# Kernel optimization log

Measured on AMD Instinct MI355X. Metric: run time of the kernel, lower is better.

The kernel has to match this reference:

```python
import math
import jax, jax.numpy as jnp
import numpy as np

N_EMBD = 768
N_HEAD = 12
BLOCK_SIZE = 1024
B, T, N_ENC = 8, 1024, 257
EPS = 1e-5


def _ln(x, g, b):
    m = jnp.mean(x, axis=-1, keepdims=True)
    v = jnp.var(x, axis=-1, keepdims=True)
    return (x - m) * jax.lax.rsqrt(v + EPS) * g + b


def _heads(t, n_head):
    B_, N_, C_ = t.shape
    return t.reshape(B_, N_, n_head, C_ // n_head).transpose(0, 2, 1, 3)  # [B,H,N,D]


def setup_inputs() -> dict:
    key = jax.random.key(0)
    ks = jax.random.split(key, 16)
    s = 0.02
    d, h4, dq = N_EMBD, 4 * N_EMBD, N_EMBD // 4
    inp = {
        'x': jax.random.normal(ks[0], (B, T, d), jnp.float32),
        'x_enc': jax.random.normal(ks[1], (B, N_ENC, d), jnp.float32),
        'ln1_g': jnp.ones((d,), jnp.float32), 'ln1_b': jnp.zeros((d,), jnp.float32),
        'ln2_g': jnp.ones((d,), jnp.float32), 'ln2_b': jnp.zeros((d,), jnp.float32),
        'ln3_g': jnp.ones((d,), jnp.float32), 'ln3_b': jnp.zeros((d,), jnp.float32),
        'attn_w': jax.random.normal(ks[2], (d, 3 * d), jnp.float32) * s,
        'attn_bias': jnp.zeros((3 * d,), jnp.float32),
        'attn_proj_w': jax.random.normal(ks[3], (d, d), jnp.float32) * s,
        'attn_proj_b': jnp.zeros((d,), jnp.float32),
        'img_w': jax.random.normal(ks[4], (d, 2 * d), jnp.float32) * s,
        'img_b': jnp.zeros((2 * d,), jnp.float32),
        'cap_w': jax.random.normal(ks[5], (d, d), jnp.float32) * s,
        'cap_b': jnp.zeros((d,), jnp.float32),
        'cross_proj_w': jax.random.normal(ks[6], (d, d), jnp.float32) * s,
        'cross_proj_b': jnp.zeros((d,), jnp.float32),
        'ad1_w': jax.random.normal(ks[7], (d, dq), jnp.float32) * s,
        'ad1_b': jnp.zeros((dq,), jnp.float32),
        'ad2_w': jax.random.normal(ks[8], (dq, d), jnp.float32) * s,
        'ad2_b': jnp.zeros((d,), jnp.float32),
        'fc_w': jax.random.normal(ks[9], (d, h4), jnp.float32) * s,
        'fc_b': jnp.zeros((h4,), jnp.float32),
        'mproj_w': jax.random.normal(ks[10], (h4, d), jnp.float32) * s,
        'mproj_b': jnp.zeros((d,), jnp.float32),
    }
    return inp


def _block(x, x_enc, ln1_g, ln1_b, ln2_g, ln2_b, ln3_g, ln3_b,
           attn_w, attn_bias, attn_proj_w, attn_proj_b,
           img_w, img_b, cap_w, cap_b, cross_proj_w, cross_proj_b,
           ad1_w, ad1_b, ad2_w, ad2_b, fc_w, fc_b, mproj_w, mproj_b):
    d, nh = N_EMBD, N_HEAD
    hd = d // nh
    scale = 1.0 / math.sqrt(hd)

    def adapter(h):
        return jax.nn.relu(h @ ad1_w + ad1_b) @ ad2_w + ad2_b

    # --- causal self-attention ---
    h = _ln(x, ln1_g, ln1_b)
    qkv = h @ attn_w + attn_bias
    q, k, v = jnp.split(qkv, 3, axis=2)
    q, k, v = _heads(q, nh), _heads(k, nh), _heads(v, nh)  # [B,H,T,hd]
    att = jnp.einsum('bhqd,bhkd->bhqk', q, k) * scale
    Tq = x.shape[1]
    causal = jnp.tril(jnp.ones((Tq, Tq), bool))
    att = jnp.where(causal, att, -jnp.inf)
    att = jax.nn.softmax(att, axis=-1)
    sa = jnp.einsum('bhqk,bhkd->bhqd', att, v).transpose(0, 2, 1, 3).reshape(x.shape)
    sa = sa @ attn_proj_w + attn_proj_b
    x = x + adapter(sa)

    # --- cross-attention (queries from x, keys/values from x_enc) ---
    hq = _ln(x, ln1_g, ln1_b)
    he = _ln(x_enc, ln3_g, ln3_b)
    kv = he @ img_w + img_b
    k2, v2 = jnp.split(kv, 2, axis=2)
    q2 = hq @ cap_w + cap_b
    q2, k2, v2 = _heads(q2, nh), _heads(k2, nh), _heads(v2, nh)
    catt = jax.nn.softmax(jnp.einsum('bhqd,bhkd->bhqk', q2, k2) * scale, axis=-1)
    ca = jnp.einsum('bhqk,bhkd->bhqd', catt, v2).transpose(0, 2, 1, 3).reshape(x.shape)
    ca = ca @ cross_proj_w + cross_proj_b
    x = x + adapter(ca)

    # --- MLP ---
    hm = _ln(x, ln2_g, ln2_b)
    m = jax.nn.gelu(hm @ fc_w + fc_b, approximate=True) @ mproj_w + mproj_b
    x = x + adapter(m)
    return x, x_enc


def reference(x, x_enc, ln1_g, ln1_b, ln2_g, ln2_b, ln3_g, ln3_b,
              attn_w, attn_bias, attn_proj_w, attn_proj_b,
              img_w, img_b, cap_w, cap_b, cross_proj_w, cross_proj_b,
              ad1_w, ad1_b, ad2_w, ad2_b, fc_w, fc_b, mproj_w, mproj_b):
    return _block(x, x_enc, ln1_g, ln1_b, ln2_g, ln2_b, ln3_g, ln3_b,
                  attn_w, attn_bias, attn_proj_w, attn_proj_b,
                  img_w, img_b, cap_w, cap_b, cross_proj_w, cross_proj_b,
                  ad1_w, ad1_b, ad2_w, ad2_b, fc_w, fc_b, mproj_w, mproj_b)
```

## Files before the change

### kernel.cpp

```cpp
#include <hip/hip_runtime.h>

typedef unsigned short u16;
typedef short bf16x8 __attribute__((ext_vector_type(8)));
typedef float f32x4 __attribute__((ext_vector_type(4)));
typedef unsigned short u16x4 __attribute__((ext_vector_type(4)));

__device__ __forceinline__ u16 f2bf(float f) {
  union { float f; unsigned u; } v; v.f = f;
  unsigned u = v.u;
  unsigned r = (u + 0x7FFFu + ((u >> 16) & 1u)) >> 16;
  return (u16)r;
}
__device__ __forceinline__ float bf2f(u16 h) {
  union { unsigned u; float f; } v; v.u = ((unsigned)h) << 16;
  return v.f;
}
__device__ __forceinline__ unsigned cvt_pk_bf16(float lo, float hi) {
  unsigned d;
  asm("v_cvt_pk_bf16_f32 %0, %1, %2" : "=v"(d) : "v"(lo), "v"(hi));
  return d;
}
__device__ __forceinline__ float gelu_f(float x) {
  const float c1 = -2.302585093f;
  const float c2 = -0.1029620967f;
  float t = __builtin_fmaf(x * x, c2, c1) * x;
  float e = exp2f(t);
  return x * __builtin_amdgcn_rcpf(e + 1.0f);
}

#define GLD_LDS16(gp, lp)                                             \
  __builtin_amdgcn_global_load_lds(                                   \
      (const __attribute__((address_space(1))) void*)(gp),            \
      (__attribute__((address_space(3))) void*)(lp), 16, 0, 0)

template<int OFF>
__device__ __forceinline__ u16x4 tr16(unsigned a) {
  u16x4 d;
  asm volatile("ds_read_b64_tr_b16 %0, %1 offset:%2" : "=&v"(d) : "v"(a), "n"(OFF));
  return d;
}
__device__ __forceinline__ bf16x8 pack8(u16x4 a, u16x4 b) {
  union { u16x4 p[2]; bf16x8 v; } u;
  u.p[0] = a; u.p[1] = b;
  return u.v;
}
__device__ __forceinline__ u16x4 pack4(unsigned w0, unsigned w1) {
  union { unsigned w[2]; u16x4 v; } u;
  u.w[0] = w0; u.w[1] = w1;
  return u.v;
}

struct TrBatch {
  const float* W[9];
  u16* Bt[9];
  int K[9], N[9], Kpad[9], Npad[9];
  int tstart[10];
};
__global__ __launch_bounds__(256)
void transpose_all(TrBatch tb) {
  __shared__ float tile[64][65];
  const int tid = blockIdx.x;
  int mi = 0;
  while (mi < 8 && tid >= tb.tstart[mi + 1]) ++mi;
  const int lt = tid - tb.tstart[mi];
  const int tx = tb.Npad[mi] >> 6;
  const int n0 = (lt % tx) * 64;
  const int k0 = (lt / tx) * 64;
  const float* W = tb.W[mi];
  u16* Bt = tb.Bt[mi];
  const int K = tb.K[mi], N = tb.N[mi], Kpad = tb.Kpad[mi];
  const int t = threadIdx.x;
  const int c = t & 63;
  const int rb = t >> 6;
#pragma unroll
  for (int i = 0; i < 16; ++i) {
    int r = i * 4 + rb;
    float v = 0.f;
    if (k0 + r < K && n0 + c < N) v = W[(size_t)(k0 + r) * N + n0 + c];
    tile[r][c] = v;
  }
  __syncthreads();
#pragma unroll
  for (int i = 0; i < 16; ++i) {
    int r = i * 4 + rb;
    Bt[(size_t)(n0 + r) * Kpad + k0 + c] = f2bf(tile[c][r]);
  }
}

__global__ __launch_bounds__(64)
void ln_kernel(const float* __restrict__ X, const float* __restrict__ G,
               const float* __restrict__ Bv, u16* __restrict__ O, int Mreal) {
  const int row = blockIdx.x;
  const int l = threadIdx.x;
  u16* op = O + (size_t)row * 768;
  if (row >= Mreal) {
    u16x4 z = {0, 0, 0, 0};
#pragma unroll
    for (int i = 0; i < 3; ++i) *(u16x4*)(op + (i * 64 + l) * 4) = z;
    return;
  }
  const float* xp = X + (size_t)row * 768;
  float v[12];
  float s = 0.f, s2 = 0.f;
#pragma unroll
  for (int i = 0; i < 3; ++i) {
    float4 t4 = *(const float4*)(xp + (i * 64 + l) * 4);
    v[i * 4 + 0] = t4.x; v[i * 4 + 1] = t4.y; v[i * 4 + 2] = t4.z; v[i * 4 + 3] = t4.w;
    s += t4.x + t4.y + t4.z + t4.w;
    s2 += t4.x * t4.x + t4.y * t4.y + t4.z * t4.z + t4.w * t4.w;
  }
#pragma unroll
  for (int off = 32; off > 0; off >>= 1) {
    s += __shfl_xor(s, off);
    s2 += __shfl_xor(s2, off);
  }
  const float mean = s * (1.0f / 768.0f);
  const float var = s2 * (1.0f / 768.0f) - mean * mean;
  const float rstd = rsqrtf(var + 1e-5f);
#pragma unroll
  for (int i = 0; i < 3; ++i) {
    int base = (i * 64 + l) * 4;
    float4 g4 = *(const float4*)(G + base);
    float4 b4 = *(const float4*)(Bv + base);
    u16x4 o4;
    o4[0] = f2bf((v[i * 4 + 0] - mean) * rstd * g4.x + b4.x);
    o4[1] = f2bf((v[i * 4 + 1] - mean) * rstd * g4.y + b4.y);
    o4[2] = f2bf((v[i * 4 + 2] - mean) * rstd * g4.z + b4.z);
    o4[3] = f2bf((v[i * 4 + 3] - mean) * rstd * g4.w + b4.w);
    *(u16x4*)(op + base) = o4;
  }
}

template<bool DOLN, bool RESID>
__global__ __launch_bounds__(64)
void resid_ln(const float* __restrict__ S, float* __restrict__ D,
              const u16* __restrict__ P,
              const float* __restrict__ G, const float* __restrict__ Bv,
              u16* __restrict__ O) {
  const int row = blockIdx.x;
  const int l = threadIdx.x;
  const float* sp = S + (size_t)row * 768;
  float* dp = D + (size_t)row * 768;
  float v[12];
  float s = 0.f, s2 = 0.f;
#pragma unroll
  for (int i = 0; i < 3; ++i) {
    const int base = (i * 64 + l) * 4;
    float4 t4 = *(const float4*)(sp + base);
    if (RESID) {
      u16x4 p4 = *(const u16x4*)(P + (size_t)row * 768 + base);
      t4.x += bf2f(p4[0]); t4.y += bf2f(p4[1]);
      t4.z += bf2f(p4[2]); t4.w += bf2f(p4[3]);
    }
    v[i * 4 + 0] = t4.x; v[i * 4 + 1] = t4.y; v[i * 4 + 2] = t4.z; v[i * 4 + 3] = t4.w;
    s += t4.x + t4.y + t4.z + t4.w;
    s2 += t4.x * t4.x + t4.y * t4.y + t4.z * t4.z + t4.w * t4.w;
    *(float4*)(dp + base) = t4;
  }
  if (DOLN) {
#pragma unroll
    for (int off = 32; off > 0; off >>= 1) {
      s += __shfl_xor(s, off);
      s2 += __shfl_xor(s2, off);
    }
    const float mean = s * (1.0f / 768.0f);
    const float var = s2 * (1.0f / 768.0f) - mean * mean;
    const float rstd = rsqrtf(var + 1e-5f);
    u16* op = O + (size_t)row * 768;
#pragma unroll
    for (int i = 0; i < 3; ++i) {
      int base = (i * 64 + l) * 4;
      float4 g4 = *(const float4*)(G + base);
      float4 b4 = *(const float4*)(Bv + base);
      u16x4 o4;
      o4[0] = f2bf((v[i * 4 + 0] - mean) * rstd * g4.x + b4.x);
      o4[1] = f2bf((v[i * 4 + 1] - mean) * rstd * g4.y + b4.y);
      o4[2] = f2bf((v[i * 4 + 2] - mean) * rstd * g4.z + b4.z);
      o4[3] = f2bf((v[i * 4 + 3] - mean) * rstd * g4.w + b4.w);
      *(u16x4*)(op + base) = o4;
    }
  }
}

template<int MODE>
__global__ void gemm_bt(const u16* __restrict__ A, const u16* __restrict__ Bt,
                        void* __restrict__ C, const float* __restrict__ bias,
                        int K, int ldc, int nbias) {
  __shared__ u16 As[2 * 128 * 32];
  __shared__ u16 Bs[2 * 128 * 32];
  const int t = threadIdx.x;
  const int lane = t & 63;
  const int wid = t >> 6;
  const int wm = (wid >> 1) * 64;
  const int wn = (wid & 1) * 64;
  const int tm = blockIdx.x * 128;
  const int tn = blockIdx.y * 128;

  f32x4 zero = {0.f, 0.f, 0.f, 0.f};
  f32x4 acc[4][4];
#pragma unroll
  for (int i = 0; i < 4; ++i)
#pragma unroll
    for (int j = 0; j < 4; ++j) acc[i][j] = zero;

  const int rowA = lane & 15;
  const int kb = (((lane >> 4) ^ ((rowA >> 1) & 3)) << 3);
  const int kTiles = K >> 6;
  for (int kt = 0; kt < kTiles; ++kt) {
    const int kk = kt << 6;
#pragma unroll
    for (int i = 0; i < 4; ++i) {
      const int c = i * 256 + t;
      const int r = (c >> 2) & 127;
      const int cc = ((c >> 9) << 5) + ((((c & 3) ^ ((r >> 1) & 3))) << 3);
      GLD_LDS16(A + (size_t)(tm + r) * K + kk + cc, As + c * 8);
      GLD_LDS16(Bt + (size_t)(tn + r) * K + kk + cc, Bs + c * 8);
    }
    __syncthreads();
#pragma unroll
    for (int ks = 0; ks < 2; ++ks) {
      bf16x8 af[4], bfr[4];
      const int base = ks * 4096;
#pragma unroll
      for (int i = 0; i < 4; ++i) {
        af[i] = *(const bf16x8*)(As + base + (wm + i * 16 + rowA) * 32 + kb);
        bfr[i] = *(const bf16x8*)(Bs + base + (wn + i * 16 + rowA) * 32 + kb);
      }
#pragma unroll
      for (int mi = 0; mi < 4; ++mi)
#pragma unroll
        for (int ni = 0; ni < 4; ++ni)
          acc[mi][ni] = __builtin_amdgcn_mfma_f32_16x16x32_bf16(af[mi], bfr[ni], acc[mi][ni], 0, 0, 0);
    }
    __syncthreads();
  }
  const int col0 = lane & 15;
  const int row0 = (lane >> 4) << 2;
#pragma unroll
  for (int mi = 0; mi < 4; ++mi) {
#pragma unroll
    for (int ni = 0; ni < 4; ++ni) {
      int col = tn + wn + ni * 16 + col0;
      float bb = (col < nbias) ? bias[col] : 0.f;
      float vv[4];
#pragma unroll
      for (int r = 0; r < 4; ++r) {
        float v = acc[mi][ni][r] + bb;
        if (MODE == 1) v = fmaxf(v, 0.f);
        else if (MODE == 2) v = gelu_f(v);
        vv[r] = v;
      }
      unsigned w0 = cvt_pk_bf16(vv[0], vv[1]);
      unsigned w1 = cvt_pk_bf16(vv[2], vv[3]);
      size_t row = (size_t)(tm + wm + mi * 16 + row0);
      u16* cp = (u16*)C + row * ldc + col;
      cp[0] = (u16)w0;
      cp[(size_t)ldc] = (u16)(w0 >> 16);
      cp[(size_t)ldc * 2] = (u16)w1;
      cp[(size_t)ldc * 3] = (u16)(w1 >> 16);
    }
  }
}

template<int MODE>
__global__ __launch_bounds__(256)
void gemm_bt_m64(const u16* __restrict__ A, const u16* __restrict__ Bt,
                 void* __restrict__ C, const float* __restrict__ bias,
                 int K, int ldc, int nbias) {
  __shared__ u16 As[2 * 64 * 32];
  __shared__ u16 Bs[2 * 128 * 32];
  const int t = threadIdx.x;
  const int lane = t & 63;
  const int wid = t >> 6;
  const int wn = wid * 32;
  const int tm = blockIdx.x * 64;
  const int tn = blockIdx.y * 128;

  f32x4 zero = {0.f, 0.f, 0.f, 0.f};
  f32x4 acc[4][2];
#pragma unroll
  for (int i = 0; i < 4; ++i)
#pragma unroll
    for (int j = 0; j < 2; ++j) acc[i][j] = zero;

  const int rowA = lane & 15;
  const int kb = (((lane >> 4) ^ ((rowA >> 1) & 3)) << 3);
  const int kTiles = K >> 6;
  for (int kt = 0; kt < kTiles; ++kt) {
    const int kk = kt << 6;
#pragma unroll
    for (int i = 0; i < 2; ++i) {
      const int c = i * 256 + t;
      const int r = (c >> 2) & 63;
      const int cc = ((c >> 8) << 5) + ((((c & 3) ^ ((r >> 1) & 3))) << 3);
      GLD_LDS16(A + (size_t)(tm + r) * K + kk + cc, As + c * 8);
    }
#pragma unroll
    for (int i = 0; i < 4; ++i) {
      const int c = i * 256 + t;
      const int r = (c >> 2) & 127;
      const int cc = ((c >> 9) << 5) + ((((c & 3) ^ ((r >> 1) & 3))) << 3);
      GLD_LDS16(Bt + (size_t)(tn + r) * K + kk + cc, Bs + c * 8);
    }
    __syncthreads();
#pragma unroll
    for (int ks = 0; ks < 2; ++ks) {
      bf16x8 af[4], bfr[2];
#pragma unroll
      for (int i = 0; i < 4; ++i)
        af[i] = *(const bf16x8*)(As + ks * 2048 + (i * 16 + rowA) * 32 + kb);
#pragma unroll
      for (int j = 0; j < 2; ++j)
        bfr[j] = *(const bf16x8*)(Bs + ks * 4096 + (wn + j * 16 + rowA) * 32 + kb);
#pragma unroll
      for (int mi = 0; mi < 4; ++mi)
#pragma unroll
        for (int ni = 0; ni < 2; ++ni)
          acc[mi][ni] = __builtin_amdgcn_mfma_f32_16x16x32_bf16(af[mi], bfr[ni], acc[mi][ni], 0, 0, 0);
    }
    __syncthreads();
  }
  const int col0 = lane & 15;
  const int row0 = (lane >> 4) << 2;
#pragma unroll
  for (int mi = 0; mi < 4; ++mi) {
#pragma unroll
    for (int ni = 0; ni < 2; ++ni) {
      int col = tn + wn + ni * 16 + col0;
      float bb = (col < nbias) ? bias[col] : 0.f;
      float vv[4];
#pragma unroll
      for (int r = 0; r < 4; ++r) {
        float v = acc[mi][ni][r] + bb;
        if (MODE == 1) v = fmaxf(v, 0.f);
        vv[r] = v;
      }
      unsigned w0 = cvt_pk_bf16(vv[0], vv[1]);
      unsigned w1 = cvt_pk_bf16(vv[2], vv[3]);
      size_t row = (size_t)(tm + mi * 16 + row0);
      u16* cp = (u16*)C + row * ldc + col;
      cp[0] = (u16)w0;
      cp[(size_t)ldc] = (u16)(w0 >> 16);
      cp[(size_t)ldc * 2] = (u16)w1;
      cp[(size_t)ldc * 3] = (u16)(w1 >> 16);
    }
  }
}

struct GemmJob {
  const u16* A; const u16* Bt; u16* C; const float* bias;
  int K, ldc, nbias, mblocks;
};
__global__ __launch_bounds__(256)
void gemm_bt_dual(GemmJob j0, GemmJob j1, int split) {
  __shared__ u16 As[2 * 128 * 32];
  __shared__ u16 Bs[2 * 128 * 32];
  const int bid = blockIdx.x;
  const GemmJob& J = (bid < split) ? j0 : j1;
  const int lb = (bid < split) ? bid : bid - split;
  const int tm = (lb % J.mblocks) * 128;
  const int tn = (lb / J.mblocks) * 128;
  const u16* A = J.A;
  const u16* Bt = J.Bt;
  const int K = J.K;

  const int t = threadIdx.x;
  const int lane = t & 63;
  const int wid = t >> 6;
  const int wm = (wid >> 1) * 64;
  const int wn = (wid & 1) * 64;

  f32x4 zero = {0.f, 0.f, 0.f, 0.f};
  f32x4 acc[4][4];
#pragma unroll
  for (int i = 0; i < 4; ++i)
#pragma unroll
    for (int j = 0; j < 4; ++j) acc[i][j] = zero;

  const int rowA = lane & 15;
  const int kb = (((lane >> 4) ^ ((rowA >> 1) & 3)) << 3);
  const int kTiles = K >> 6;
  for (int kt = 0; kt < kTiles; ++kt) {
    const int kk = kt << 6;
#pragma unroll
    for (int i = 0; i < 4; ++i) {
      const int c = i * 256 + t;
      const int r = (c >> 2) & 127;
      const int cc = ((c >> 9) << 5) + ((((c & 3) ^ ((r >> 1) & 3))) << 3);
      GLD_LDS16(A + (size_t)(tm + r) * K + kk + cc, As + c * 8);
      GLD_LDS16(Bt + (size_t)(tn + r) * K + kk + cc, Bs + c * 8);
    }
    __syncthreads();
#pragma unroll
    for (int ks = 0; ks < 2; ++ks) {
      bf16x8 af[4], bfr[4];
      const int base = ks * 4096;
#pragma unroll
      for (int i = 0; i < 4; ++i) {
        af[i] = *(const bf16x8*)(As + base + (wm + i * 16 + rowA) * 32 + kb);
        bfr[i] = *(const bf16x8*)(Bs + base + (wn + i * 16 + rowA) * 32 + kb);
      }
#pragma unroll
      for (int mi = 0; mi < 4; ++mi)
#pragma unroll
        for (int ni = 0; ni < 4; ++ni)
          acc[mi][ni] = __builtin_amdgcn_mfma_f32_16x16x32_bf16(af[mi], bfr[ni], acc[mi][ni], 0, 0, 0);
    }
    __syncthreads();
  }
  const int col0 = lane & 15;
  const int row0 = (lane >> 4) << 2;
#pragma unroll
  for (int mi = 0; mi < 4; ++mi) {
#pragma unroll
    for (int ni = 0; ni < 4; ++ni) {
      int col = tn + wn + ni * 16 + col0;
      float bb = (col < J.nbias) ? J.bias[col] : 0.f;
      unsigned w0 = cvt_pk_bf16(acc[mi][ni][0] + bb, acc[mi][ni][1] + bb);
      unsigned w1 = cvt_pk_bf16(acc[mi][ni][2] + bb, acc[mi][ni][3] + bb);
      size_t row = (size_t)(tm + wm + mi * 16 + row0);
      u16* cp = J.C + row * J.ldc + col;
      cp[0] = (u16)w0;
      cp[(size_t)J.ldc] = (u16)(w0 >> 16);
      cp[(size_t)J.ldc * 2] = (u16)w1;
      cp[(size_t)J.ldc * 3] = (u16)(w1 >> 16);
    }
  }
}

template<bool CAUSAL>
__global__ __launch_bounds__(256)
void attn_mfma(const u16* __restrict__ Q, const u16* __restrict__ Kp,
               const u16* __restrict__ Vp,
               u16* __restrict__ O0, u16* __restrict__ O1, float2* __restrict__ ML,
               int seqkv, int qrs, int krs,
               long long qBatch, long long kBatch,
               int qoff, int koff, int voff) {
  __shared__ __align__(16) u16 Ks[64 * 64];
  __shared__ __align__(16) u16 Vs[4096];
  __shared__ __align__(16) u16 Ps[4][1024];
  const int t = threadIdx.x;
  const int lane = t & 63;
  const int wid = t >> 6;
  const int b = blockIdx.x / 12, h = blockIdx.x % 12;
  const int yq = CAUSAL ? ((int)gridDim.y - 1 - (int)blockIdx.y) : (int)blockIdx.y;
  const int q0 = yq * 64;
  const int colid = lane & 15;
  const int rgrp = lane >> 4;
  const int z = CAUSAL ? blockIdx.z : 0;

  int kt_begin = 0, kt_end;
  if (CAUSAL) {
    const int ntr = yq + 1;
    const int half = (ntr + 1) >> 1;
    kt_begin = z ? half : 0;
    kt_end = z ? ntr : half;
  } else {
    kt_end = (seqkv + 63) >> 6;
  }
  u16* Op = (CAUSAL && z) ? O1 : O0;

  if (CAUSAL && kt_begin >= kt_end) {
    if (colid == 0) {
#pragma unroll
      for (int r = 0; r < 4; ++r) {
        int qrow = q0 + wid * 16 + rgrp * 4 + r;
        ML[((size_t)z * 8192 + b * 1024 + qrow) * 12 + h] = make_float2(-1e30f, 0.f);
      }
    }
    return;
  }

  const u16* qp = Q + (size_t)b * qBatch + qoff + (size_t)(q0 + wid * 16 + colid) * qrs + h * 64;
  bf16x8 qa[2];
#pragma unroll
  for (int s = 0; s < 2; ++s) qa[s] = *(const bf16x8*)(qp + s * 32 + (rgrp << 3));

  f32x4 oacc[4];
#pragma unroll
  for (int i = 0; i < 4; ++i) oacc[i] = (f32x4){0.f, 0.f, 0.f, 0.f};
  float m[4] = {-1e30f, -1e30f, -1e30f, -1e30f};
  float l[4] = {0.f, 0.f, 0.f, 0.f};

  const u16* kbase = Kp + (size_t)b * kBatch + koff + h * 64;
  const u16* vbase = Vp + (size_t)b * kBatch + voff + h * 64;

  const int srr = t >> 3, sdc = t & 7;
  int kwo[2], vwo[2];
#pragma unroll
  for (int i = 0; i < 2; ++i) {
    const int r = srr + 32 * i;
    kwo[i] = r * 64 + ((sdc ^ (r & 7)) << 3);
    vwo[i] = ((sdc >> 1) << 10) + (i << 9) + (((srr >> 2) & 1) << 8)
           + (((srr >> 3) & 3) << 6) + ((srr & 3) << 4) + (((2 * sdc) & 3) << 2);
  }
  const unsigned vs_base = (unsigned)(size_t)&Vs[0] + 8u * (unsigned)lane;
  const unsigned ps_base = (unsigned)(size_t)&Ps[wid][0] + 8u * (unsigned)lane;

  bf16x8 kz[2], vz[2];
  auto LOADT = [&](int kt) {
    const int k0 = kt * 64;
#pragma unroll
    for (int i = 0; i < 2; ++i) {
      const int tk = k0 + srr + 32 * i;
      const int dc = sdc << 3;
      kz[i] = (bf16x8){0, 0, 0, 0, 0, 0, 0, 0};
      vz[i] = (bf16x8){0, 0, 0, 0, 0, 0, 0, 0};
      if (tk < seqkv) {
        kz[i] = *(const bf16x8*)(kbase + (size_t)tk * krs + dc);
        vz[i] = *(const bf16x8*)(vbase + (size_t)tk * krs + dc);
      }
    }
  };
  LOADT(kt_begin);

  constexpr float SC2 = 0.18033688011112042f;

  for (int kt = kt_begin; kt < kt_end; ++kt) {
    const int k0 = kt * 64;
#pragma unroll
    for (int i = 0; i < 2; ++i) {
      *(bf16x8*)&Ks[kwo[i]] = kz[i];
      *(bf16x8*)&Vs[vwo[i]] = vz[i];
    }
    __syncthreads();
    if (kt + 1 < kt_end) LOADT(kt + 1);

    f32x4 sacc[4];
#pragma unroll
    for (int c = 0; c < 4; ++c) sacc[c] = (f32x4){0.f, 0.f, 0.f, 0.f};
#pragma unroll
    for (int c = 0; c < 4; ++c)
#pragma unroll
      for (int s = 0; s < 2; ++s) {
        bf16x8 kf = *(const bf16x8*)&Ks[(c * 16 + colid) * 64 +
                                        ((((s << 2) + rgrp) ^ (colid & 7)) << 3)];
        sacc[c] = __builtin_amdgcn_mfma_f32_16x16x32_bf16(qa[s], kf, sacc[c], 0, 0, 0);
      }

    const bool domask = CAUSAL ? (kt == yq) : (kt == kt_end - 1);
    if (domask) {
#pragma unroll
      for (int c = 0; c < 4; ++c) {
        int kv = k0 + c * 16 + colid;
#pragma unroll
        for (int r = 0; r < 4; ++r) {
          int q = q0 + wid * 16 + rgrp * 4 + r;
          if ((CAUSAL && kv > q) || (!CAUSAL && kv >= seqkv)) sacc[c][r] = -1e30f;
        }
      }
    }

    float pms[4];
#pragma unroll
    for (int r = 0; r < 4; ++r) {
      float v = fmaxf(fmaxf(sacc[0][r], sacc[1][r]), fmaxf(sacc[2][r], sacc[3][r]));
#pragma unroll
      for (int off = 1; off < 16; off <<= 1) v = fmaxf(v, __shfl_xor(v, off));
      pms[r] = v * SC2;
    }
    bool ok = (pms[0] <= m[0] + 8.f) && (pms[1] <= m[1] + 8.f) &&
              (pms[2] <= m[2] + 8.f) && (pms[3] <= m[3] + 8.f);
    if (!__all(ok)) {
#pragma unroll
      for (int r = 0; r < 4; ++r) {
        float newm = fmaxf(m[r], pms[r]);
        float corr = exp2f(m[r] - newm);
        m[r] = newm;
        l[r] *= corr;
#pragma unroll
        for (int dc2 = 0; dc2 < 4; ++dc2) oacc[dc2][r] *= corr;
      }
    }

    float pv[4][4];
    float psum[4] = {0.f, 0.f, 0.f, 0.f};
#pragma unroll
    for (int c = 0; c < 4; ++c)
#pragma unroll
      for (int r = 0; r < 4; ++r) {
        float p = exp2f(__builtin_fmaf(sacc[c][r], SC2, -m[r]));
        pv[c][r] = p;
        psum[r] += p;
      }
#pragma unroll
    for (int r = 0; r < 4; ++r) {
#pragma unroll
      for (int off = 1; off < 16; off <<= 1) psum[r] += __shfl_xor(psum[r], off);
      l[r] += psum[r];
    }

#pragma unroll
    for (int c = 0; c < 4; ++c) {
      unsigned w0 = cvt_pk_bf16(pv[c][0], pv[c][1]);
      unsigned w1 = cvt_pk_bf16(pv[c][2], pv[c][3]);
      const int pa = ((c >> 1) << 9) + (((colid >> 2) & 1) << 8)
                   + (((2 * c + (colid >> 3)) & 3) << 6) + ((colid & 3) << 4) + (rgrp << 2);
      *(u16x4*)&Ps[wid][pa] = pack4(w0, w1);
    }
    __builtin_amdgcn_sched_barrier(0);

    u16x4 p00 = tr16<0>(ps_base);
    u16x4 p01 = tr16<512>(ps_base);
    u16x4 p10 = tr16<1024>(ps_base);
    u16x4 p11 = tr16<1536>(ps_base);
    asm volatile("s_waitcnt lgkmcnt(0)" ::: "memory");
    __builtin_amdgcn_sched_barrier(0);
    bf16x8 pf0 = pack8(p00, p01);
    bf16x8 pf1 = pack8(p10, p11);

#pragma unroll
    for (int dc2 = 0; dc2 < 4; ++dc2) {
      const unsigned va = vs_base + (unsigned)(dc2 * 2048);
      u16x4 v00 = tr16<0>(va);
      u16x4 v01 = tr16<512>(va);
      u16x4 v10 = tr16<1024>(va);
      u16x4 v11 = tr16<1536>(va);
      asm volatile("s_waitcnt lgkmcnt(0)" ::: "memory");
      __builtin_amdgcn_sched_barrier(0);
      bf16x8 vf0 = pack8(v00, v01);
      bf16x8 vf1 = pack8(v10, v11);
      oacc[dc2] = __builtin_amdgcn_mfma_f32_16x16x32_bf16(pf0, vf0, oacc[dc2], 0, 0, 0);
      oacc[dc2] = __builtin_amdgcn_mfma_f32_16x16x32_bf16(pf1, vf1, oacc[dc2], 0, 0, 0);
    }
    __syncthreads();
  }

#pragma unroll
  for (int r = 0; r < 4; ++r) {
    int qrow = q0 + wid * 16 + rgrp * 4 + r;
    u16* op = Op + ((size_t)b * 1024 + qrow) * 768 + h * 64;
    if (CAUSAL) {
      unsigned w0 = cvt_pk_bf16(oacc[0][r], oacc[1][r]);
      unsigned w1 = cvt_pk_bf16(oacc[2][r], oacc[3][r]);
      op[colid] = (u16)w0;
      op[16 + colid] = (u16)(w0 >> 16);
      op[32 + colid] = (u16)w1;
      op[48 + colid] = (u16)(w1 >> 16);
      if (colid == 0)
        ML[((size_t)z * 8192 + b * 1024 + qrow) * 12 + h] = make_float2(m[r], l[r]);
    } else {
      float inv = 1.f / l[r];
      unsigned w0 = cvt_pk_bf16(oacc[0][r] * inv, oacc[1][r] * inv);
      unsigned w1 = cvt_pk_bf16(oacc[2][r] * inv, oacc[3][r] * inv);
      op[colid] = (u16)w0;
      op[16 + colid] = (u16)(w0 >> 16);
      op[32 + colid] = (u16)w1;
      op[48 + colid] = (u16)(w1 >> 16);
    }
  }
}

__global__ __launch_bounds__(64)
void attn_combine(const u16* __restrict__ P0, const u16* __restrict__ P1,
                  const float2* __restrict__ ML, u16* __restrict__ O) {
  const int row = blockIdx.x;
  const int l = threadIdx.x;
#pragma unroll
  for (int i = 0; i < 3; ++i) {
    const int base = (i * 64 + l) * 4;
    const int h = base >> 6;
    float2 ml0 = ML[(size_t)row * 12 + h];
    float2 ml1 = ML[(size_t)8192 * 12 + row * 12 + h];
    float mm = fmaxf(ml0.x, ml1.x);
    float w0 = exp2f(ml0.x - mm);
    float w1 = exp2f(ml1.x - mm);
    float inv = 1.f / (ml0.y * w0 + ml1.y * w1);
    u16x4 a = *(const u16x4*)(P0 + (size_t)row * 768 + base);
    u16x4 c = *(const u16x4*)(P1 + (size_t)row * 768 + base);
    u16x4 o4;
#pragma unroll
    for (int j = 0; j < 4; ++j)
      o4[j] = f2bf((bf2f(a[j]) * w0 + bf2f(c[j]) * w1) * inv);
    *(u16x4*)(O + (size_t)row * 768 + base) = o4;
  }
}

extern "C" void kernel_launch(void* const* d_in, const int* in_sizes, int n_in,
                              void* d_out, int out_size, void* d_ws, size_t ws_size,
                              hipStream_t stream) {
  const float* x        = (const float*)d_in[0];
  const float* x_enc    = (const float*)d_in[1];
  const float* ln1_g    = (const float*)d_in[2];
  const float* ln1_b    = (const float*)d_in[3];
  const float* ln2_g    = (const float*)d_in[4];
  const float* ln2_b    = (const float*)d_in[5];
  const float* ln3_g    = (const float*)d_in[6];
  const float* ln3_b    = (const float*)d_in[7];
  const float* attn_w   = (const float*)d_in[8];
  const float* attn_bias= (const float*)d_in[9];
  const float* proj_w   = (const float*)d_in[10];
  const float* proj_b   = (const float*)d_in[11];
  const float* img_w    = (const float*)d_in[12];
  const float* img_b    = (const float*)d_in[13];
  const float* cap_w    = (const float*)d_in[14];
  const float* cap_b    = (const float*)d_in[15];
  const float* cross_w  = (const float*)d_in[16];
  const float* cross_b  = (const float*)d_in[17];
  const float* ad1_w    = (const float*)d_in[18];
  const float* ad1_b    = (const float*)d_in[19];
  const float* ad2_w    = (const float*)d_in[20];
  const float* ad2_b    = (const float*)d_in[21];
  const float* fc_w     = (const float*)d_in[22];
  const float* fc_b     = (const float*)d_in[23];
  const float* mproj_w  = (const float*)d_in[24];
  const float* mproj_b  = (const float*)d_in[25];

  const int Mx = 8192;
  const int Me = 2056;
  const int MeP = 2176;

  float* out_x  = (float*)d_out;
  float* out_xe = out_x + (size_t)Mx * 768;

  char* ws = (char*)d_ws;
  size_t off = 0;
  auto alloc = [&](size_t elems) {
    u16* p = (u16*)(ws + off);
    off = (off + elems * 2 + 255) & ~(size_t)255;
    return p;
  };
  u16* wt_attn  = alloc((size_t)2304 * 768);
  u16* wt_proj  = alloc((size_t)768 * 768);
  u16* wt_img   = alloc((size_t)1536 * 768);
  u16* wt_cap   = alloc((size_t)768 * 768);
  u16* wt_cross = alloc((size_t)768 * 768);
  u16* wt_ad1   = alloc((size_t)256 * 768);
  u16* wt_ad2   = alloc((size_t)768 * 256);
  u16* wt_fc    = alloc((size_t)3072 * 768);
  u16* wt_mproj = alloc((size_t)768 * 3072);
  u16* hbuf     = alloc((size_t)Mx * 768);
  u16* big      = alloc((size_t)Mx * 3072);
  u16* p0       = alloc((size_t)Mx * 768);
  u16* p1       = alloc((size_t)Mx * 768);
  u16* hid      = alloc((size_t)Mx * 256);
  float2* mlbuf = (float2*)alloc((size_t)2 * 8192 * 12 * 4);
  u16* q2  = big;
  u16* kvb = big + (size_t)Mx * 768;

  hipMemcpyAsync(out_xe, x_enc, (size_t)Me * 768 * 4, hipMemcpyDeviceToDevice, stream);

  TrBatch tb;
  int nt = 0;
  tb.tstart[0] = 0;
  auto addT = [&](const float* W, u16* Bt, int K, int N, int Kp, int Np) {
    tb.W[nt] = W; tb.Bt[nt] = Bt; tb.K[nt] = K; tb.N[nt] = N;
    tb.Kpad[nt] = Kp; tb.Npad[nt] = Np;
    tb.tstart[nt + 1] = tb.tstart[nt] + (Np / 64) * (Kp / 64);
    ++nt;
  };
  addT(attn_w, wt_attn, 768, 2304, 768, 2304);
  addT(proj_w, wt_proj, 768, 768, 768, 768);
  addT(img_w, wt_img, 768, 1536, 768, 1536);
  addT(cap_w, wt_cap, 768, 768, 768, 768);
  addT(cross_w, wt_cross, 768, 768, 768, 768);
  addT(ad1_w, wt_ad1, 768, 192, 768, 256);
  addT(ad2_w, wt_ad2, 192, 768, 256, 768);
  addT(fc_w, wt_fc, 768, 3072, 768, 3072);
  addT(mproj_w, wt_mproj, 3072, 768, 3072, 768);
  transpose_all<<<tb.tstart[9], 256, 0, stream>>>(tb);

  auto GEMM = [&](const u16* A, const u16* Bt, void* C, const float* bias,
                  int M, int N, int K, int ldc, int nbias, int mode) {
    dim3 g(M / 128, N / 128);
    if (mode == 0)      gemm_bt<0><<<g, 256, 0, stream>>>(A, Bt, C, bias, K, ldc, nbias);
    else if (mode == 1) gemm_bt<1><<<g, 256, 0, stream>>>(A, Bt, C, bias, K, ldc, nbias);
    else                gemm_bt<2><<<g, 256, 0, stream>>>(A, Bt, C, bias, K, ldc, nbias);
  };
  auto GEMM_M64 = [&](const u16* A, const u16* Bt, void* C, const float* bias,
                      int M, int N, int K, int ldc, int nbias, int mode) {
    dim3 g(M / 64, N / 128);
    if (mode == 0) gemm_bt_m64<0><<<g, 256, 0, stream>>>(A, Bt, C, bias, K, ldc, nbias);
    else           gemm_bt_m64<1><<<g, 256, 0, stream>>>(A, Bt, C, bias, K, ldc, nbias);
  };
  auto ADAPTER = [&](const u16* in, u16* padw) {
    GEMM_M64(in, wt_ad1, hid, ad1_b, Mx, 256, 768, 256, 192, 1);
    GEMM_M64(hid, wt_ad2, padw, ad2_b, Mx, 768, 256, 768, 768, 0);
  };

  resid_ln<true, false><<<Mx, 64, 0, stream>>>(x, out_x, nullptr, ln1_g, ln1_b, hbuf);

  GEMM(hbuf, wt_attn, big, attn_bias, Mx, 2304, 768, 2304, 2304, 0);
  attn_mfma<true><<<dim3(96, 16, 2), 256, 0, stream>>>(
      big, big, big, hbuf, p1, mlbuf, 1024, 2304, 2304,
      (long long)1024 * 2304, (long long)1024 * 2304, 0, 768, 1536);
  attn_combine<<<Mx, 64, 0, stream>>>(hbuf, p1, mlbuf, p0);
  GEMM_M64(p0, wt_proj, p1, proj_b, Mx, 768, 768, 768, 768, 0);
  ADAPTER(p1, p0);
  resid_ln<true, true><<<Mx, 64, 0, stream>>>(out_x, out_x, p0, ln1_g, ln1_b, hbuf);

  ln_kernel<<<MeP, 64, 0, stream>>>(x_enc, ln3_g, ln3_b, p0, Me);
  {
    GemmJob jkv = { p0,   wt_img, kvb, img_b, 768, 1536, 1536, MeP / 128 };
    GemmJob jq2 = { hbuf, wt_cap, q2,  cap_b, 768, 768,  768,  Mx / 128 };
    const int split = (MeP / 128) * (1536 / 128);
    const int total = split + (Mx / 128) * (768 / 128);
    gemm_bt_dual<<<total, 256, 0, stream>>>(jkv, jq2, split);
  }
  attn_mfma<false><<<dim3(96, 16), 256, 0, stream>>>(
      q2, kvb, kvb, p1, nullptr, nullptr, 257, 768, 1536,
      (long long)1024 * 768, (long long)257 * 1536, 0, 0, 768);
  GEMM_M64(p1, wt_cross, p0, cross_b, Mx, 768, 768, 768, 768, 0);
  ADAPTER(p0, p1);
  resid_ln<true, true><<<Mx, 64, 0, stream>>>(out_x, out_x, p1, ln2_g, ln2_b, hbuf);

  GEMM(hbuf, wt_fc, big, fc_b, Mx, 3072, 768, 3072, 3072, 2);
  GEMM_M64(big, wt_mproj, p0, mproj_b, Mx, 768, 3072, 768, 768, 0);
  ADAPTER(p0, p1);
  resid_ln<false, true><<<Mx, 64, 0, stream>>>(out_x, out_x, p1, nullptr, nullptr, nullptr);

  (void)in_sizes; (void)n_in; (void)out_size; (void)ws_size;
}
```

Before: 449.2 us.

## Drop causal split-KV and combine kernel; compute row sums via MFMA

Removes the two-way KV split of causal attention and the separate combine kernel, so each block handles the whole causal range for its query tile and normalizes in place. It also replaces the shuffle-based softmax row-sum reduction with an MFMA against a ones vector. This saves the combine kernel launch, the partial-output and m/l traffic, and the shuffles. In exchange the grid is halved, which risks imbalance across causal tiles and lower occupancy on the long tiles. The row sums are now taken from bf16-rounded probabilities, which changes numerics slightly.

```diff
diff --git a/kernel.cpp b/kernel.cpp
--- a/kernel.cpp
+++ b/kernel.cpp
@@ -431,8 +431,7 @@
 template<bool CAUSAL>
 __global__ __launch_bounds__(256)
 void attn_mfma(const u16* __restrict__ Q, const u16* __restrict__ Kp,
-               const u16* __restrict__ Vp,
-               u16* __restrict__ O0, u16* __restrict__ O1, float2* __restrict__ ML,
+               const u16* __restrict__ Vp, u16* __restrict__ O,
                int seqkv, int qrs, int krs,
                long long qBatch, long long kBatch,
                int qoff, int koff, int voff) {
@@ -447,29 +446,8 @@
   const int q0 = yq * 64;
   const int colid = lane & 15;
   const int rgrp = lane >> 4;
-  const int z = CAUSAL ? blockIdx.z : 0;
-
-  int kt_begin = 0, kt_end;
-  if (CAUSAL) {
-    const int ntr = yq + 1;
-    const int half = (ntr + 1) >> 1;
-    kt_begin = z ? half : 0;
-    kt_end = z ? ntr : half;
-  } else {
-    kt_end = (seqkv + 63) >> 6;
-  }
-  u16* Op = (CAUSAL && z) ? O1 : O0;
-
-  if (CAUSAL && kt_begin >= kt_end) {
-    if (colid == 0) {
-#pragma unroll
-      for (int r = 0; r < 4; ++r) {
-        int qrow = q0 + wid * 16 + rgrp * 4 + r;
-        ML[((size_t)z * 8192 + b * 1024 + qrow) * 12 + h] = make_float2(-1e30f, 0.f);
-      }
-    }
-    return;
-  }
+
+  const int kt_end = CAUSAL ? (yq + 1) : ((seqkv + 63) >> 6);
 
   const u16* qp = Q + (size_t)b * qBatch + qoff + (size_t)(q0 + wid * 16 + colid) * qrs + h * 64;
   bf16x8 qa[2];
@@ -481,6 +459,9 @@
   for (int i = 0; i < 4; ++i) oacc[i] = (f32x4){0.f, 0.f, 0.f, 0.f};
   float m[4] = {-1e30f, -1e30f, -1e30f, -1e30f};
   float l[4] = {0.f, 0.f, 0.f, 0.f};
+
+  const u16x4 one4 = {0x3F80, 0x3F80, 0x3F80, 0x3F80};
+  const bf16x8 ones8 = pack8(one4, one4);
 
   const u16* kbase = Kp + (size_t)b * kBatch + koff + h * 64;
   const u16* vbase = Vp + (size_t)b * kBatch + voff + h * 64;
@@ -512,11 +493,11 @@
       }
     }
   };
-  LOADT(kt_begin);
+  LOADT(0);
 
   constexpr float SC2 = 0.18033688011112042f;
 
-  for (int kt = kt_begin; kt < kt_end; ++kt) {
+  for (int kt = 0; kt < kt_end; ++kt) {
     const int k0 = kt * 64;
 #pragma unroll
     for (int i = 0; i < 2; ++i) {
@@ -574,21 +555,11 @@
     }
 
     float pv[4][4];
-    float psum[4] = {0.f, 0.f, 0.f, 0.f};
 #pragma unroll
     for (int c = 0; c < 4; ++c)
 #pragma unroll
-      for (int r = 0; r < 4; ++r) {
-        float p = exp2f(__builtin_fmaf(sacc[c][r], SC2, -m[r]));
-        pv[c][r] = p;
-        psum[r] += p;
-      }
-#pragma unroll
-    for (int r = 0; r < 4; ++r) {
-#pragma unroll
-      for (int off = 1; off < 16; off <<= 1) psum[r] += __shfl_xor(psum[r], off);
-      l[r] += psum[r];
-    }
+      for (int r = 0; r < 4; ++r)
+        pv[c][r] = exp2f(__builtin_fmaf(sacc[c][r], SC2, -m[r]));
 
 #pragma unroll
     for (int c = 0; c < 4; ++c) {
@@ -608,6 +579,10 @@
     __builtin_amdgcn_sched_barrier(0);
     bf16x8 pf0 = pack8(p00, p01);
     bf16x8 pf1 = pack8(p10, p11);
+
+    f32x4 sum_acc = (f32x4){0.f, 0.f, 0.f, 0.f};
+    sum_acc = __builtin_amdgcn_mfma_f32_16x16x32_bf16(pf0, ones8, sum_acc, 0, 0, 0);
+    sum_acc = __builtin_amdgcn_mfma_f32_16x16x32_bf16(pf1, ones8, sum_acc, 0, 0, 0);
 
 #pragma unroll
     for (int dc2 = 0; dc2 < 4; ++dc2) {
@@ -623,56 +598,22 @@
       oacc[dc2] = __builtin_amdgcn_mfma_f32_16x16x32_bf16(pf0, vf0, oacc[dc2], 0, 0, 0);
       oacc[dc2] = __builtin_amdgcn_mfma_f32_16x16x32_bf16(pf1, vf1, oacc[dc2], 0, 0, 0);
     }
+#pragma unroll
+    for (int r = 0; r < 4; ++r) l[r] += sum_acc[r];
     __syncthreads();
   }
 
 #pragma unroll
   for (int r = 0; r < 4; ++r) {
     int qrow = q0 + wid * 16 + rgrp * 4 + r;
-    u16* op = Op + ((size_t)b * 1024 + qrow) * 768 + h * 64;
-    if (CAUSAL) {
-      unsigned w0 = cvt_pk_bf16(oacc[0][r], oacc[1][r]);
-      unsigned w1 = cvt_pk_bf16(oacc[2][r], oacc[3][r]);
-      op[colid] = (u16)w0;
-      op[16 + colid] = (u16)(w0 >> 16);
-      op[32 + colid] = (u16)w1;
-      op[48 + colid] = (u16)(w1 >> 16);
-      if (colid == 0)
-        ML[((size_t)z * 8192 + b * 1024 + qrow) * 12 + h] = make_float2(m[r], l[r]);
-    } else {
-      float inv = 1.f / l[r];
-      unsigned w0 = cvt_pk_bf16(oacc[0][r] * inv, oacc[1][r] * inv);
-      unsigned w1 = cvt_pk_bf16(oacc[2][r] * inv, oacc[3][r] * inv);
-      op[colid] = (u16)w0;
-      op[16 + colid] = (u16)(w0 >> 16);
-      op[32 + colid] = (u16)w1;
-      op[48 + colid] = (u16)(w1 >> 16);
-    }
-  }
-}
-
-__global__ __launch_bounds__(64)
-void attn_combine(const u16* __restrict__ P0, const u16* __restrict__ P1,
-                  const float2* __restrict__ ML, u16* __restrict__ O) {
-  const int row = blockIdx.x;
-  const int l = threadIdx.x;
-#pragma unroll
-  for (int i = 0; i < 3; ++i) {
-    const int base = (i * 64 + l) * 4;
-    const int h = base >> 6;
-    float2 ml0 = ML[(size_t)row * 12 + h];
-    float2 ml1 = ML[(size_t)8192 * 12 + row * 12 + h];
-    float mm = fmaxf(ml0.x, ml1.x);
-    float w0 = exp2f(ml0.x - mm);
-    float w1 = exp2f(ml1.x - mm);
-    float inv = 1.f / (ml0.y * w0 + ml1.y * w1);
-    u16x4 a = *(const u16x4*)(P0 + (size_t)row * 768 + base);
-    u16x4 c = *(const u16x4*)(P1 + (size_t)row * 768 + base);
-    u16x4 o4;
-#pragma unroll
-    for (int j = 0; j < 4; ++j)
-      o4[j] = f2bf((bf2f(a[j]) * w0 + bf2f(c[j]) * w1) * inv);
-    *(u16x4*)(O + (size_t)row * 768 + base) = o4;
+    u16* op = O + ((size_t)b * 1024 + qrow) * 768 + h * 64;
+    float inv = 1.f / l[r];
+    unsigned w0 = cvt_pk_bf16(oacc[0][r] * inv, oacc[1][r] * inv);
+    unsigned w1 = cvt_pk_bf16(oacc[2][r] * inv, oacc[3][r] * inv);
+    op[colid] = (u16)w0;
+    op[16 + colid] = (u16)(w0 >> 16);
+    op[32 + colid] = (u16)w1;
+    op[48 + colid] = (u16)(w1 >> 16);
   }
 }
 
@@ -734,7 +675,6 @@
   u16* p0       = alloc((size_t)Mx * 768);
   u16* p1       = alloc((size_t)Mx * 768);
   u16* hid      = alloc((size_t)Mx * 256);
-  float2* mlbuf = (float2*)alloc((size_t)2 * 8192 * 12 * 4);
   u16* q2  = big;
   u16* kvb = big + (size_t)Mx * 768;
 
@@ -781,10 +721,9 @@
   resid_ln<true, false><<<Mx, 64, 0, stream>>>(x, out_x, nullptr, ln1_g, ln1_b, hbuf);
 
   GEMM(hbuf, wt_attn, big, attn_bias, Mx, 2304, 768, 2304, 2304, 0);
-  attn_mfma<true><<<dim3(96, 16, 2), 256, 0, stream>>>(
-      big, big, big, hbuf, p1, mlbuf, 1024, 2304, 2304,
+  attn_mfma<true><<<dim3(96, 16), 256, 0, stream>>>(
+      big, big, big, p0, 1024, 2304, 2304,
       (long long)1024 * 2304, (long long)1024 * 2304, 0, 768, 1536);
-  attn_combine<<<Mx, 64, 0, stream>>>(hbuf, p1, mlbuf, p0);
   GEMM_M64(p0, wt_proj, p1, proj_b, Mx, 768, 768, 768, 768, 0);
   ADAPTER(p1, p0);
   resid_ln<true, true><<<Mx, 64, 0, stream>>>(out_x, out_x, p0, ln1_g, ln1_b, hbuf);
@@ -798,7 +737,7 @@
     gemm_bt_dual<<<total, 256, 0, stream>>>(jkv, jq2, split);
   }
   attn_mfma<false><<<dim3(96, 16), 256, 0, stream>>>(
-      q2, kvb, kvb, p1, nullptr, nullptr, 257, 768, 1536,
+      q2, kvb, kvb, p1, 257, 768, 1536,
       (long long)1024 * 768, (long long)257 * 1536, 0, 0, 768);
   GEMM_M64(p1, wt_cross, p0, cross_b, Mx, 768, 768, 768, 768, 0);
   ADAPTER(p0, p1);
```

After: 436.6 us. 1.03x faster.
